# Optimization experiments

Measured on AMD Instinct MI355X. Metric: run time of the kernel, lower is better.

The kernel has to match this reference:

```python
import jax, jax.numpy as jnp
import numpy as np

B, S, T, V, D = 32, 64, 512, 50257, 128


def setup_inputs() -> dict:
    key = jax.random.key(0)
    k1, k2, k3 = jax.random.split(key, 3)
    word_encs = jax.random.randint(k1, (B, T), 0, V, dtype=jnp.int32)
    span_idxs = jnp.sort(
        jax.random.randint(k2, (B, S, 2), 0, T + 1, dtype=jnp.int32), axis=-1
    )
    W = jax.random.normal(k3, (V, D), dtype=jnp.float32) * 0.02
    b = jnp.zeros((D,), dtype=jnp.float32)
    return {"word_encs": word_encs, "span_idxs": span_idxs, "W": W, "b": b}


def reference(word_encs, span_idxs, W, b):
    # word_encs: [B, T] int word ids; span_idxs: [B, S, 2] (i, j) with i<=j
    Bn, Tn = word_encs.shape
    Sn = span_idxs.shape[1]
    Vn = W.shape[0]
    t = jnp.arange(Tn)
    i = span_idxs[..., 0:1]  # [B, S, 1]
    j = span_idxs[..., 1:2]  # [B, S, 1]
    in_span = (t[None, None, :] >= i) & (t[None, None, :] < j)  # [B, S, T]
    # route out-of-span tokens to a dump slot Vn, then drop it
    ids = jnp.where(in_span, word_encs[:, None, :], Vn)  # [B, S, T]
    bow = jnp.zeros((Bn, Sn, Vn + 1), dtype=W.dtype)
    bow = bow.at[
        jnp.arange(Bn)[:, None, None], jnp.arange(Sn)[None, :, None], ids
    ].set(1.0)
    bow = bow[:, :, :Vn]  # multi-hot [B, S, V]
    return bow @ W + b  # dim reduction: [B, S, D]
```

## Files before the change

### kernel.cpp

```cpp
#include <hip/hip_runtime.h>

#define BB 32
#define SS 64
#define TT 512
#define VV 50257
#define DD 128

#define DSLICES 4
#define DW (DD / DSLICES)
#define NCH 32
#define CHL (TT / NCH)
#define NTHREADS (NCH * DW)
#define NSLOT (TT / 4 + 2)

__global__ __launch_bounds__(NTHREADS) void fused_bow(
    const int* __restrict__ tok,
    const int* __restrict__ spans,
    const float* __restrict__ W,
    const float* __restrict__ bias,
    float* __restrict__ out)
{
    const int b     = blockIdx.x >> 2;
    const int dbase = (blockIdx.x & 3) * DW;
    const int tid   = threadIdx.x;
    const int c     = tid >> 5;
    const int d     = tid & (DW - 1);

    __shared__ alignas(16) int tokS[TT];
    __shared__ int spanI[SS], spanJ[SS];
    __shared__ unsigned char isB[TT + 1];
    __shared__ int flagScan[TT + 1];
    __shared__ short slot[TT + 1];
    __shared__ float csum[NCH][DW];
    __shared__ int dupT[TT], dupP[TT], dupV[TT];
    __shared__ int ndup;
    __shared__ float PB[NSLOT][DW];

    if (tid < TT) tokS[tid] = tok[b * TT + tid];
    if (tid < SS) {
        spanI[tid] = spans[(b * SS + tid) * 2 + 0];
        spanJ[tid] = spans[(b * SS + tid) * 2 + 1];
    }
    if (tid <= TT) { isB[tid] = 0; flagScan[tid] = 0; }
    if (tid == 0) ndup = 0;
    __syncthreads();

    if (tid < SS) {
        isB[spanI[tid]] = 1;  flagScan[spanI[tid]] = 1;
        isB[spanJ[tid]] = 1;  flagScan[spanJ[tid]] = 1;
    }
    __syncthreads();

    const int myflag = (tid <= TT) ? flagScan[tid] : 0;
    for (int off = 1; off <= TT; off <<= 1) {
        int v = 0;
        if (tid <= TT && tid >= off) v = flagScan[tid - off];
        __syncthreads();
        if (tid <= TT) flagScan[tid] += v;
        __syncthreads();
    }
    if (tid <= TT) slot[tid] = (short)(flagScan[tid] - myflag);

    if (tid < TT) {
        const int t = tid, v = tokS[t];
        const int4* rowv = reinterpret_cast<const int4*>(tokS);
        int p = -1;
        const int n4 = (t + 3) >> 2;
        for (int u4 = 0; u4 < n4; ++u4) {
            const int4 q = rowv[u4];
            const int base = u4 << 2;
            if (base + 0 < t && q.x == v) p = base + 0;
            if (base + 1 < t && q.y == v) p = base + 1;
            if (base + 2 < t && q.z == v) p = base + 2;
            if (base + 3 < t && q.w == v) p = base + 3;
        }
        if (p >= 0) {
            const int k = atomicAdd(&ndup, 1);
            dupT[k] = t; dupP[k] = p; dupV[k] = v;
        }
    }

    const float* Wd = W + dbase;
    const int tbase = c * CHL;
    float acc = 0.f;
#pragma unroll
    for (int t = 0; t < CHL; ++t)
        acc += Wd[(size_t)tokS[tbase + t] * DD + d];
    csum[c][d] = acc;
    __syncthreads();

    float off = 0.f;
    for (int cc = 0; cc < c; ++cc) off += csum[cc][d];
    if (tid < DW && isB[0]) PB[0][tid] = 0.f;

    acc = off;
#pragma unroll
    for (int t = 0; t < CHL; ++t) {
        acc += Wd[(size_t)tokS[tbase + t] * DD + d];
        const int p = tbase + t + 1;
        if (isB[p]) PB[slot[p]][d] = acc;
    }
    __syncthreads();

    const int nd = ndup;
    const float bv = bias[dbase + d];
    for (int s = c; s < SS; s += NCH) {
        const int i = spanI[s], j = spanJ[s];
        float r = PB[slot[j]][d] - PB[slot[i]][d] + bv;
        for (int k = 0; k < nd; ++k) {
            if (dupT[k] < j && dupP[k] >= i)
                r -= Wd[(size_t)dupV[k] * DD + d];
        }
        out[(size_t)(b * SS + s) * DD + dbase + d] = r;
    }
}

extern "C" void kernel_launch(void* const* d_in, const int* in_sizes, int n_in,
                              void* d_out, int out_size, void* d_ws, size_t ws_size,
                              hipStream_t stream) {
    const int*   word_encs = (const int*)  d_in[0];
    const int*   span_idxs = (const int*)  d_in[1];
    const float* W         = (const float*)d_in[2];
    const float* bias      = (const float*)d_in[3];
    float*       out       = (float*)      d_out;

    fused_bow<<<BB * DSLICES, NTHREADS, 0, stream>>>(word_encs, span_idxs, W, bias, out);
}
```

Before: 96.55 us.

## Use bitmask popcount slots, hash dedup, and single-pass prefix over finer D slices

Splits D into 8 slices with 64 chunks so each thread handles fewer tokens across twice as many blocks. The log-step scan over boundary flags becomes a popcount over a bitmask. The quadratic backward search for duplicate tokens is gated by a shared hash of first occurrence. W is gathered once into per-thread register prefixes, and chunk offsets are added to boundary slots in a separate pass, so the second gather of W is gone. This adds more shared memory (the hash table), atomics and an extra pass, and caps duplicates at 512.

```diff
diff --git a/kernel.cpp b/kernel.cpp
--- a/kernel.cpp
+++ b/kernel.cpp
@@ -6,12 +6,15 @@
 #define VV 50257
 #define DD 128
 
-#define DSLICES 4
+#define DSLICES 8
 #define DW (DD / DSLICES)
-#define NCH 32
+#define NCH 64
 #define CHL (TT / NCH)
 #define NTHREADS (NCH * DW)
-#define NSLOT (TT / 4 + 2)
+#define NSLOT 130
+#define NWORDS 17
+#define HSIZE 4096
+#define MAXDUP 512
 
 __global__ __launch_bounds__(NTHREADS) void fused_bow(
     const int* __restrict__ tok,
@@ -20,19 +23,21 @@
     const float* __restrict__ bias,
     float* __restrict__ out)
 {
-    const int b     = blockIdx.x >> 2;
-    const int dbase = (blockIdx.x & 3) * DW;
+    const int b     = blockIdx.x >> 3;
+    const int dbase = (blockIdx.x & 7) * DW;
     const int tid   = threadIdx.x;
-    const int c     = tid >> 5;
+    const int c     = tid >> 4;
     const int d     = tid & (DW - 1);
 
     __shared__ alignas(16) int tokS[TT];
     __shared__ int spanI[SS], spanJ[SS];
-    __shared__ unsigned char isB[TT + 1];
-    __shared__ int flagScan[TT + 1];
+    __shared__ unsigned int words[NWORDS];
     __shared__ short slot[TT + 1];
+    __shared__ short posOfSlot[NSLOT];
     __shared__ float csum[NCH][DW];
-    __shared__ int dupT[TT], dupP[TT], dupV[TT];
+    __shared__ float coff[NCH][DW];
+    __shared__ unsigned int hashT[HSIZE];
+    __shared__ int dupT[MAXDUP], dupP[MAXDUP], dupV[MAXDUP];
     __shared__ int ndup;
     __shared__ float PB[NSLOT][DW];
 
@@ -41,76 +46,88 @@
         spanI[tid] = spans[(b * SS + tid) * 2 + 0];
         spanJ[tid] = spans[(b * SS + tid) * 2 + 1];
     }
-    if (tid <= TT) { isB[tid] = 0; flagScan[tid] = 0; }
+    if (tid < NWORDS) words[tid] = 0u;
+    if (tid < NSLOT) posOfSlot[tid] = 0;
     if (tid == 0) ndup = 0;
+    for (int h = tid; h < HSIZE; h += NTHREADS) hashT[h] = 0xFFFFFFFFu;
     __syncthreads();
 
     if (tid < SS) {
-        isB[spanI[tid]] = 1;  flagScan[spanI[tid]] = 1;
-        isB[spanJ[tid]] = 1;  flagScan[spanJ[tid]] = 1;
+        const int i = spanI[tid], j = spanJ[tid];
+        atomicOr(&words[i >> 5], 1u << (i & 31));
+        atomicOr(&words[j >> 5], 1u << (j & 31));
+    }
+    if (tid < TT) {
+        const unsigned int h = ((unsigned int)tokS[tid] * 2654435761u) >> 20;
+        atomicMin(&hashT[h], (unsigned int)tid);
     }
     __syncthreads();
 
-    const int myflag = (tid <= TT) ? flagScan[tid] : 0;
-    for (int off = 1; off <= TT; off <<= 1) {
-        int v = 0;
-        if (tid <= TT && tid >= off) v = flagScan[tid - off];
-        __syncthreads();
-        if (tid <= TT) flagScan[tid] += v;
-        __syncthreads();
+    if (tid <= TT) {
+        const int wt = tid >> 5;
+        int s = 0;
+        for (int w = 0; w < wt; ++w) s += __popc(words[w]);
+        s += __popc(words[wt] & ((1u << (tid & 31)) - 1u));
+        slot[tid] = (short)s;
+        if ((words[wt] >> (tid & 31)) & 1u) posOfSlot[s] = (short)tid;
     }
-    if (tid <= TT) slot[tid] = (short)(flagScan[tid] - myflag);
-
     if (tid < TT) {
-        const int t = tid, v = tokS[t];
-        const int4* rowv = reinterpret_cast<const int4*>(tokS);
-        int p = -1;
-        const int n4 = (t + 3) >> 2;
-        for (int u4 = 0; u4 < n4; ++u4) {
-            const int4 q = rowv[u4];
-            const int base = u4 << 2;
-            if (base + 0 < t && q.x == v) p = base + 0;
-            if (base + 1 < t && q.y == v) p = base + 1;
-            if (base + 2 < t && q.z == v) p = base + 2;
-            if (base + 3 < t && q.w == v) p = base + 3;
-        }
-        if (p >= 0) {
-            const int k = atomicAdd(&ndup, 1);
-            dupT[k] = t; dupP[k] = p; dupV[k] = v;
+        const int v = tokS[tid];
+        const unsigned int h = ((unsigned int)v * 2654435761u) >> 20;
+        if (hashT[h] < (unsigned int)tid) {
+            int p = -1;
+            for (int u = tid - 1; u >= 0; --u)
+                if (tokS[u] == v) { p = u; break; }
+            if (p >= 0) {
+                const int k = atomicAdd(&ndup, 1);
+                dupT[k] = tid; dupP[k] = p; dupV[k] = v;
+            }
         }
     }
-
     const float* Wd = W + dbase;
     const int tbase = c * CHL;
-    float acc = 0.f;
+    float pref[CHL];
+    {
+        float acc = 0.f;
 #pragma unroll
-    for (int t = 0; t < CHL; ++t)
-        acc += Wd[(size_t)tokS[tbase + t] * DD + d];
-    csum[c][d] = acc;
+        for (int t = 0; t < CHL; ++t) {
+            acc += Wd[(size_t)tokS[tbase + t] * DD + d];
+            pref[t] = acc;
+        }
+        csum[c][d] = acc;
+    }
     __syncthreads();
 
-    float off = 0.f;
-    for (int cc = 0; cc < c; ++cc) off += csum[cc][d];
-    if (tid < DW && isB[0]) PB[0][tid] = 0.f;
-
-    acc = off;
+    {
+        float o = 0.f;
+        for (int cc = 0; cc < c; ++cc) o += csum[cc][d];
+        coff[c][d] = o;
+    }
 #pragma unroll
     for (int t = 0; t < CHL; ++t) {
-        acc += Wd[(size_t)tokS[tbase + t] * DD + d];
         const int p = tbase + t + 1;
-        if (isB[p]) PB[slot[p]][d] = acc;
+        if ((words[p >> 5] >> (p & 31)) & 1u)
+            PB[slot[p]][d] = pref[t];
+    }
+    if (tid < DW && (words[0] & 1u)) PB[0][tid] = 0.f;
+    __syncthreads();
+
+    for (int idx = tid; idx < NSLOT * DW; idx += NTHREADS) {
+        const int k = idx >> 4, dd = idx & (DW - 1);
+        const int p = posOfSlot[k];
+        if (p > 0) PB[k][dd] += coff[(p - 1) >> 3][dd];
     }
     __syncthreads();
 
     const int nd = ndup;
     const float bv = bias[dbase + d];
-    for (int s = c; s < SS; s += NCH) {
+    {
+        const int s = c;
         const int i = spanI[s], j = spanJ[s];
         float r = PB[slot[j]][d] - PB[slot[i]][d] + bv;
-        for (int k = 0; k < nd; ++k) {
+        for (int k = 0; k < nd; ++k)
             if (dupT[k] < j && dupP[k] >= i)
                 r -= Wd[(size_t)dupV[k] * DD + d];
-        }
         out[(size_t)(b * SS + s) * DD + dbase + d] = r;
     }
 }
```

Result: slower. 120.1 us (+24.4%).
